# Kernel tuning notes

Hardware: AMD Instinct MI355X
Metric: run time of the kernel (lower is better)

The kernel has to match this reference:

```python
import jax, jax.numpy as jnp
import numpy as np

N, D, E = 16384, 256, 8
H = D // 2  # gate hidden


def setup_inputs() -> dict:
    key = jax.random.key(0)
    ks = jax.random.split(key, 10)
    s = lambda fan_in: 1.0 / np.sqrt(fan_in)
    return {
        "x":   jax.random.normal(ks[0], (N, D), dtype=jnp.float32),
        # gate: Linear(D, D//2) -> ReLU -> Linear(D//2, E) -> Softmax
        "Wg1": jax.random.uniform(ks[1], (D, H), jnp.float32, -s(D), s(D)),
        "bg1": jax.random.uniform(ks[2], (H,), jnp.float32, -s(D), s(D)),
        "Wg2": jax.random.uniform(ks[3], (H, E), jnp.float32, -s(H), s(H)),
        "bg2": jax.random.uniform(ks[4], (E,), jnp.float32, -s(H), s(H)),
        # experts: per-expert Linear(D,D) -> ReLU -> (Dropout eval=identity) -> Linear(D,D)
        "W1": jax.random.uniform(ks[5], (E, D, D), jnp.float32, -s(D), s(D)),
        "b1": jax.random.uniform(ks[6], (E, D), jnp.float32, -s(D), s(D)),
        "W2": jax.random.uniform(ks[7], (E, D, D), jnp.float32, -s(D), s(D)),
        "b2": jax.random.uniform(ks[8], (E, D), jnp.float32, -s(D), s(D)),
    }


def reference(x, Wg1, bg1, Wg2, bg2, W1, b1, W2, b2):
    # gate: [N, E] softmax over experts
    g = jax.nn.softmax(jax.nn.relu(x @ Wg1 + bg1) @ Wg2 + bg2, axis=-1)
    # all experts applied densely via batched GEMMs (fuses the Python loop)
    h = jax.nn.relu(jnp.einsum("nd,edh->neh", x, W1) + b1)  # [N, E, D]
    y = jnp.einsum("neh,ehd->ned", h, W2) + b2              # [N, E, D]
    # weighted combine: sum_e g[n,e] * y[n,e,:]
    return jnp.einsum("ned,ne->nd", y, g)
```

## Files before the change

### kernel.cpp

```cpp
#include <hip/hip_runtime.h>


typedef unsigned short USH;
typedef float f32x4 __attribute__((ext_vector_type(4)));
typedef __bf16 bf16x8 __attribute__((ext_vector_type(8)));

#define AS1 __attribute__((address_space(1)))
#define AS3 __attribute__((address_space(3)))

__device__ __forceinline__ USH f2bf(float f) {
  unsigned int u = __float_as_uint(f);
  u += 0x7fffu + ((u >> 16) & 1u);
  return (USH)(u >> 16);
}

__device__ __forceinline__ void gl2lds16(const void* g, void* l) {
  __builtin_amdgcn_global_load_lds((AS1 const void*)g, (AS3 void*)l, 16, 0, 0);
}


__global__ __launch_bounds__(256) void k_prep(
    const float* __restrict__ x,
    const float* __restrict__ Wg1,
    const float* __restrict__ W1,
    const float* __restrict__ W2,
    USH* __restrict__ xb, USH* __restrict__ wg1t,
    USH* __restrict__ w1f, USH* __restrict__ w2f) {
  __shared__ float T[64][65];
  int b = blockIdx.x, tid = threadIdx.x;

  if (b < 2048) {
    size_t i8 = ((size_t)b * 256 + tid) * 8;
    float4 a = *(const float4*)(x + i8);
    float4 c = *(const float4*)(x + i8 + 4);
    USH v[8];
    v[0] = f2bf(a.x); v[1] = f2bf(a.y); v[2] = f2bf(a.z); v[3] = f2bf(a.w);
    v[4] = f2bf(c.x); v[5] = f2bf(c.y); v[6] = f2bf(c.z); v[7] = f2bf(c.w);
    *(uint4*)(xb + i8) = *(const uint4*)v;
  } else if (b < 2176) {
    int bp = b - 2048;
    int e = bp >> 4, tl = bp & 15;
    int c0 = (tl >> 2) * 64, h0 = (tl & 3) * 64;
    const float* src = W1 + (size_t)e * 65536;
#pragma unroll
    for (int p = 0; p < 4; ++p) {
      int r = p * 16 + (tid >> 4), d4 = (tid & 15) * 4;
      float4 v = *(const float4*)(src + (size_t)(c0 + r) * 256 + h0 + d4);
      T[r][d4] = v.x; T[r][d4 + 1] = v.y; T[r][d4 + 2] = v.z; T[r][d4 + 3] = v.w;
    }
    __syncthreads();
#pragma unroll
    for (int p = 0; p < 4; ++p) {
      int hr = p * 16 + (tid >> 4), c4 = (tid & 15) * 4;
      USH w[4];
#pragma unroll
      for (int j = 0; j < 4; ++j) w[j] = f2bf(T[c4 + j][hr]);
      int h = h0 + hr;
      int t = h >> 4, lh = h & 15;
      int kt = c0 >> 6, ch = c4 >> 5, q = (c4 >> 3) & 3, u0 = c4 & 7;
      size_t idx = ((size_t)((e * 64 + kt * 16 + t) * 2 + ch)) * 512 + (q * 16 + lh) * 8 + u0;
      *(uint2*)(w1f + idx) = *(const uint2*)w;
    }
  } else if (b < 2184) {
    int bp = b - 2176;
    int c0 = (bp >> 1) * 64, h0 = (bp & 1) * 64;
#pragma unroll
    for (int p = 0; p < 4; ++p) {
      int r = p * 16 + (tid >> 4), d4 = (tid & 15) * 4;
      float4 v = *(const float4*)(Wg1 + (size_t)(c0 + r) * 128 + h0 + d4);
      T[r][d4] = v.x; T[r][d4 + 1] = v.y; T[r][d4 + 2] = v.z; T[r][d4 + 3] = v.w;
    }
    __syncthreads();
#pragma unroll
    for (int p = 0; p < 4; ++p) {
      int hr = p * 16 + (tid >> 4), c4 = (tid & 15) * 4;
      USH w[4];
#pragma unroll
      for (int j = 0; j < 4; ++j) w[j] = f2bf(T[c4 + j][hr]);
      *(uint2*)(wg1t + (size_t)(h0 + hr) * 256 + c0 + c4) = *(const uint2*)w;
    }
  } else {
    int bp = b - 2184;
    int e = bp >> 4, tl = bp & 15;
    int h0 = (tl >> 2) * 64, d0 = (tl & 3) * 64;
    const float* src = W2 + (size_t)e * 65536;
#pragma unroll
    for (int p = 0; p < 4; ++p) {
      int r = p * 16 + (tid >> 4), d4 = (tid & 15) * 4;
      float4 v = *(const float4*)(src + (size_t)(h0 + r) * 256 + d0 + d4);
      T[r][d4] = v.x; T[r][d4 + 1] = v.y; T[r][d4 + 2] = v.z; T[r][d4 + 3] = v.w;
    }
    __syncthreads();
#pragma unroll
    for (int p = 0; p < 4; ++p) {
      int dr = p * 16 + (tid >> 4), h4 = (tid & 15) * 4;
      USH w[4];
#pragma unroll
      for (int j = 0; j < 4; ++j) w[j] = f2bf(T[h4 + j][dr]);
      int d = d0 + dr;
      int t = d >> 4, ld = d & 15;
      int ht = h0 >> 6, ch = h4 >> 5, q = (h4 >> 3) & 3, u0 = h4 & 7;
      size_t idx = ((size_t)((e * 64 + ht * 16 + t) * 2 + ch)) * 512 + (q * 16 + ld) * 8 + u0;
      *(uint2*)(w2f + idx) = *(const uint2*)w;
    }
  }
}


__global__ __launch_bounds__(256) void k_gate(const USH* __restrict__ xb,
                                              const USH* __restrict__ wg1t,
                                              const float* __restrict__ bg1,
                                              const float* __restrict__ wg2,
                                              const float* __restrict__ bg2,
                                              float* __restrict__ g) {
  __shared__ __align__(16) USH As[32 * 64];
  __shared__ __align__(16) USH Bs[128 * 64];
  __shared__ float hg[32 * 129];
  __shared__ float bg1s[128];
  __shared__ float w2s[128 * 8];
  __shared__ float b2s[8];
  __shared__ float lg[32 * 8];

  int tid = threadIdx.x;
  int wave = tid >> 6, lane = tid & 63;
  int quad = lane >> 4, l16 = lane & 15;
  int sw = l16 & 7;
  int wr = wave >> 1, wc = wave & 1;
  int rowBase = blockIdx.x * 32;

  for (int t = tid; t < 1024; t += 256) w2s[t] = wg2[t];
  if (tid < 8) b2s[tid] = bg2[tid];
  if (tid < 128) bg1s[tid] = bg1[tid];

  f32x4 acc[4] = {};
  for (int kt = 0; kt < 4; ++kt) {
    int kb = kt * 64;
    {
      int r = tid >> 3, c8 = (tid & 7) ^ (r & 7);
      gl2lds16(xb + (size_t)(rowBase + r) * 256 + kb + c8 * 8, As + (size_t)tid * 8);
    }
#pragma unroll
    for (int c = 0; c < 4; ++c) {
      int i = c * 256 + tid;
      int r = i >> 3, c8 = (i & 7) ^ (r & 7);
      gl2lds16(wg1t + (size_t)r * 256 + kb + c8 * 8, Bs + (size_t)i * 8);
    }
    __syncthreads();
#pragma unroll
    for (int kkc = 0; kkc < 8; kkc += 4) {
      bf16x8 av = *(const bf16x8*)(As + (wr * 16 + l16) * 64 + (((kkc + quad) ^ sw) * 8));
#pragma unroll
      for (int j = 0; j < 4; ++j) {
        bf16x8 bv = *(const bf16x8*)(Bs + (wc * 64 + j * 16 + l16) * 64 + (((kkc + quad) ^ sw) * 8));
        acc[j] = __builtin_amdgcn_mfma_f32_16x16x32_bf16(av, bv, acc[j], 0, 0, 0);
      }
    }
    __syncthreads();
  }

#pragma unroll
  for (int j = 0; j < 4; ++j)
#pragma unroll
    for (int r = 0; r < 4; ++r) {
      int row = wr * 16 + quad * 4 + r;
      int col = wc * 64 + j * 16 + l16;
      hg[row * 129 + col] = fmaxf(acc[j][r] + bg1s[col], 0.0f);
    }
  __syncthreads();

  {
    int row = tid >> 3, p = tid & 7;
    float s = b2s[p];
    for (int k = 0; k < 128; ++k) s += hg[row * 129 + k] * w2s[k * 8 + p];
    lg[row * 8 + p] = s;
  }
  __syncthreads();

  if (tid < 32) {
    float l[8];
    float m = -1e30f;
#pragma unroll
    for (int e = 0; e < 8; ++e) { l[e] = lg[tid * 8 + e]; m = fmaxf(m, l[e]); }
    float s = 0.0f;
#pragma unroll
    for (int e = 0; e < 8; ++e) { l[e] = expf(l[e] - m); s += l[e]; }
    float inv = 1.0f / s;
    size_t grow = rowBase + tid;
#pragma unroll
    for (int e = 0; e < 8; ++e) g[grow * 8 + e] = l[e] * inv;
  }
}


__global__ __launch_bounds__(512) void k_moe(const USH* __restrict__ xb,
                                             const USH* __restrict__ w1f,
                                             const USH* __restrict__ w2f,
                                             const float* __restrict__ b1,
                                             const float* __restrict__ b2,
                                             const float* __restrict__ g,
                                             float* __restrict__ out) {
  __shared__ __align__(16) USH xs[4 * 64 * 64];
  __shared__ __align__(16) USH Hs[2][64 * 256];
  __shared__ float b1s[2048];
  __shared__ float b2s[2048];
  __shared__ float gse[512];

  int tid = threadIdx.x;
  int wave = tid >> 6, lane = tid & 63;
  int quad = lane >> 4, l16 = lane & 15;
  int sw = l16 & 7;
  int rowBase = blockIdx.x * 64;

#pragma unroll
  for (int it = 0; it < 4; ++it) {
    int i = it * 512 + tid;
    int kt = i >> 9, rem = i & 511;
    int r = rem >> 3, slot = rem & 7;
    int c8 = slot ^ (r & 7);
    gl2lds16(xb + (size_t)(rowBase + r) * 256 + kt * 64 + c8 * 8, xs + (size_t)i * 8);
  }

  bf16x8 wra[8], wrb[8];
  auto LDWH = [&](bf16x8* dst, const USH* We, int tb) {
#pragma unroll
    for (int k = 0; k < 2; ++k)
#pragma unroll
      for (int c = 0; c < 2; ++c)
#pragma unroll
        for (int i = 0; i < 2; ++i)
          dst[k * 4 + c * 2 + i] = *(const bf16x8*)(
              We + (size_t)(((tb + k) * 16 + wave * 2 + i) * 2 + c) * 512 + lane * 8);
  };
  LDWH(wra, w1f, 0);
  LDWH(wrb, w1f, 2);

#pragma unroll
  for (int t = 0; t < 4; ++t) {
    b1s[t * 512 + tid] = b1[t * 512 + tid];
    b2s[t * 512 + tid] = b2[t * 512 + tid];
  }
  {
    int e = tid >> 6, n = tid & 63;
    gse[tid] = g[(size_t)(rowBase + n) * 8 + e];
  }

  asm volatile("s_waitcnt vmcnt(0) lgkmcnt(0)" ::: "memory");
  __builtin_amdgcn_s_barrier();

  f32x4 oacc[4][2] = {};

#pragma unroll 1
  for (int e = 0; e < 8; ++e) {
    const USH* W2e = w2f + (size_t)e * 65536;
    const USH* W1n = w1f + (size_t)((e + 1) & 7) * 65536;
    f32x4 hacc[2][4] = {};

#pragma unroll
    for (int kt = 0; kt < 2; ++kt)
#pragma unroll
      for (int c = 0; c < 2; ++c) {
        int cs = ((c * 4 + quad) ^ sw) * 8;
        bf16x8 bv[4];
#pragma unroll
        for (int j = 0; j < 4; ++j)
          bv[j] = *(const bf16x8*)(xs + kt * 4096 + (j * 16 + l16) * 64 + cs);
#pragma unroll
        for (int i = 0; i < 2; ++i)
#pragma unroll
          for (int j = 0; j < 4; ++j)
            hacc[i][j] = __builtin_amdgcn_mfma_f32_16x16x32_bf16(
                wra[kt * 4 + c * 2 + i], bv[j], hacc[i][j], 0, 0, 0);
      }
    LDWH(wra, W2e, 0);
#pragma unroll
    for (int kt = 2; kt < 4; ++kt)
#pragma unroll
      for (int c = 0; c < 2; ++c) {
        int cs = ((c * 4 + quad) ^ sw) * 8;
        bf16x8 bv[4];
#pragma unroll
        for (int j = 0; j < 4; ++j)
          bv[j] = *(const bf16x8*)(xs + kt * 4096 + (j * 16 + l16) * 64 + cs);
#pragma unroll
        for (int i = 0; i < 2; ++i)
#pragma unroll
          for (int j = 0; j < 4; ++j)
            hacc[i][j] = __builtin_amdgcn_mfma_f32_16x16x32_bf16(
                wrb[(kt - 2) * 4 + c * 2 + i], bv[j], hacc[i][j], 0, 0, 0);
      }
    LDWH(wrb, W2e, 2);

    USH* Hb = &Hs[e & 1][0];
#pragma unroll
    for (int i = 0; i < 2; ++i) {
      int slot = (wave & 1) * 4 + i * 2 + (quad >> 1);
      int hb = wave * 32 + i * 16 + quad * 4;
#pragma unroll
      for (int j = 0; j < 4; ++j) {
        int n = j * 16 + l16;
        float gg = gse[e * 64 + n];
        USH w4[4];
#pragma unroll
        for (int r = 0; r < 4; ++r)
          w4[r] = f2bf(fmaxf(hacc[i][j][r] + b1s[e * 256 + hb + r], 0.0f) * gg);
        int off = n * 256 + (wave >> 1) * 64 + ((slot ^ (n & 7)) * 8) + (quad & 1) * 4;
        *(uint2*)(Hb + off) = *(const uint2*)w4;
      }
    }

    asm volatile("s_waitcnt lgkmcnt(0)" ::: "memory");
    __builtin_amdgcn_s_barrier();

#pragma unroll
    for (int ht = 0; ht < 2; ++ht)
#pragma unroll
      for (int c = 0; c < 2; ++c) {
        int cs = ((c * 4 + quad) ^ sw) * 8;
        bf16x8 av[4];
#pragma unroll
        for (int i = 0; i < 4; ++i)
          av[i] = *(const bf16x8*)(Hb + (i * 16 + l16) * 256 + ht * 64 + cs);
#pragma unroll
        for (int i = 0; i < 4; ++i)
#pragma unroll
          for (int j = 0; j < 2; ++j)
            oacc[i][j] = __builtin_amdgcn_mfma_f32_16x16x32_bf16(
                av[i], wra[ht * 4 + c * 2 + j], oacc[i][j], 0, 0, 0);
      }
    LDWH(wra, W1n, 0);
#pragma unroll
    for (int ht = 2; ht < 4; ++ht)
#pragma unroll
      for (int c = 0; c < 2; ++c) {
        int cs = ((c * 4 + quad) ^ sw) * 8;
        bf16x8 av[4];
#pragma unroll
        for (int i = 0; i < 4; ++i)
          av[i] = *(const bf16x8*)(Hb + (i * 16 + l16) * 256 + ht * 64 + cs);
#pragma unroll
        for (int i = 0; i < 4; ++i)
#pragma unroll
          for (int j = 0; j < 2; ++j)
            oacc[i][j] = __builtin_amdgcn_mfma_f32_16x16x32_bf16(
                av[i], wrb[(ht - 2) * 4 + c * 2 + j], oacc[i][j], 0, 0, 0);
      }
    LDWH(wrb, W1n, 2);
  }

#pragma unroll
  for (int i = 0; i < 4; ++i)
#pragma unroll
    for (int r = 0; r < 4; ++r) {
      int n = i * 16 + quad * 4 + r;
      size_t grow = (size_t)(rowBase + n) * 256;
#pragma unroll
      for (int j = 0; j < 2; ++j) {
        int d = wave * 32 + j * 16 + l16;
        float bias = 0.0f;
#pragma unroll
        for (int ee = 0; ee < 8; ++ee) bias += gse[ee * 64 + n] * b2s[ee * 256 + d];
        out[grow + d] = oacc[i][j][r] + bias;
      }
    }
}


extern "C" void kernel_launch(void* const* d_in, const int* in_sizes, int n_in,
                              void* d_out, int out_size, void* d_ws, size_t ws_size,
                              hipStream_t stream) {
  const float* x   = (const float*)d_in[0];
  const float* Wg1 = (const float*)d_in[1];
  const float* bg1 = (const float*)d_in[2];
  const float* Wg2 = (const float*)d_in[3];
  const float* bg2 = (const float*)d_in[4];
  const float* W1  = (const float*)d_in[5];
  const float* b1  = (const float*)d_in[6];
  const float* W2  = (const float*)d_in[7];
  const float* b2  = (const float*)d_in[8];
  float* out = (float*)d_out;

  char* ws = (char*)d_ws;
  USH*   xb  = (USH*)(ws);
  USH*   w1f = (USH*)(ws + 8388608);
  USH*   wg1t = (USH*)(ws + 9437184);
  USH*   w2f = (USH*)(ws + 9502720);
  float* g   = (float*)(ws + 10584064);

  hipLaunchKernelGGL(k_prep, dim3(2312), dim3(256), 0, stream,
                     x, Wg1, W1, W2, xb, wg1t, w1f, w2f);
  hipLaunchKernelGGL(k_gate, dim3(512), dim3(256), 0, stream,
                     xb, wg1t, bg1, Wg2, bg2, g);
  hipLaunchKernelGGL(k_moe, dim3(256), dim3(512), 0, stream,
                     xb, w1f, w2f, b1, b2, g, out);
}
```

Measured before the change: 130.6 us.

## Fuse gate network and x bf16 conversion into the MoE kernel

Result: faster. 123.2 us (-5.7%).

```diff
diff --git a/kernel.cpp b/kernel.cpp
--- a/kernel.cpp
+++ b/kernel.cpp
@@ -4,9 +4,6 @@
 typedef unsigned short USH;
 typedef float f32x4 __attribute__((ext_vector_type(4)));
 typedef __bf16 bf16x8 __attribute__((ext_vector_type(8)));
-
-#define AS1 __attribute__((address_space(1)))
-#define AS3 __attribute__((address_space(3)))
 
 __device__ __forceinline__ USH f2bf(float f) {
   unsigned int u = __float_as_uint(f);
@@ -14,32 +11,17 @@
   return (USH)(u >> 16);
 }
 
-__device__ __forceinline__ void gl2lds16(const void* g, void* l) {
-  __builtin_amdgcn_global_load_lds((AS1 const void*)g, (AS3 void*)l, 16, 0, 0);
-}
-
 
 __global__ __launch_bounds__(256) void k_prep(
-    const float* __restrict__ x,
     const float* __restrict__ Wg1,
     const float* __restrict__ W1,
     const float* __restrict__ W2,
-    USH* __restrict__ xb, USH* __restrict__ wg1t,
-    USH* __restrict__ w1f, USH* __restrict__ w2f) {
+    USH* __restrict__ w1f, USH* __restrict__ w2f, USH* __restrict__ wg1f) {
   __shared__ float T[64][65];
   int b = blockIdx.x, tid = threadIdx.x;
 
-  if (b < 2048) {
-    size_t i8 = ((size_t)b * 256 + tid) * 8;
-    float4 a = *(const float4*)(x + i8);
-    float4 c = *(const float4*)(x + i8 + 4);
-    USH v[8];
-    v[0] = f2bf(a.x); v[1] = f2bf(a.y); v[2] = f2bf(a.z); v[3] = f2bf(a.w);
-    v[4] = f2bf(c.x); v[5] = f2bf(c.y); v[6] = f2bf(c.z); v[7] = f2bf(c.w);
-    *(uint4*)(xb + i8) = *(const uint4*)v;
-  } else if (b < 2176) {
-    int bp = b - 2048;
-    int e = bp >> 4, tl = bp & 15;
+  if (b < 128) {
+    int e = b >> 4, tl = b & 15;
     int c0 = (tl >> 2) * 64, h0 = (tl & 3) * 64;
     const float* src = W1 + (size_t)e * 65536;
 #pragma unroll
@@ -57,12 +39,36 @@
       for (int j = 0; j < 4; ++j) w[j] = f2bf(T[c4 + j][hr]);
       int h = h0 + hr;
       int t = h >> 4, lh = h & 15;
-      int kt = c0 >> 6, ch = c4 >> 5, q = (c4 >> 3) & 3, u0 = c4 & 7;
+      int kt = c0 >> 6, ch = (c4 >> 5) & 1, q = (c4 >> 3) & 3, u0 = c4 & 7;
       size_t idx = ((size_t)((e * 64 + kt * 16 + t) * 2 + ch)) * 512 + (q * 16 + lh) * 8 + u0;
       *(uint2*)(w1f + idx) = *(const uint2*)w;
     }
-  } else if (b < 2184) {
-    int bp = b - 2176;
+  } else if (b < 256) {
+    int bp = b - 128;
+    int e = bp >> 4, tl = bp & 15;
+    int h0 = (tl >> 2) * 64, d0 = (tl & 3) * 64;
+    const float* src = W2 + (size_t)e * 65536;
+#pragma unroll
+    for (int p = 0; p < 4; ++p) {
+      int r = p * 16 + (tid >> 4), d4 = (tid & 15) * 4;
+      float4 v = *(const float4*)(src + (size_t)(h0 + r) * 256 + d0 + d4);
+      T[r][d4] = v.x; T[r][d4 + 1] = v.y; T[r][d4 + 2] = v.z; T[r][d4 + 3] = v.w;
+    }
+    __syncthreads();
+#pragma unroll
+    for (int p = 0; p < 4; ++p) {
+      int dr = p * 16 + (tid >> 4), h4 = (tid & 15) * 4;
+      USH w[4];
+#pragma unroll
+      for (int j = 0; j < 4; ++j) w[j] = f2bf(T[h4 + j][dr]);
+      int d = d0 + dr;
+      int t = d >> 4, ld = d & 15;
+      int ht = h0 >> 6, ch = (h4 >> 5) & 1, q = (h4 >> 3) & 3, u0 = h4 & 7;
+      size_t idx = ((size_t)((e * 64 + ht * 16 + t) * 2 + ch)) * 512 + (q * 16 + ld) * 8 + u0;
+      *(uint2*)(w2f + idx) = *(const uint2*)w;
+    }
+  } else {
+    int bp = b - 256;
     int c0 = (bp >> 1) * 64, h0 = (bp & 1) * 64;
 #pragma unroll
     for (int p = 0; p < 4; ++p) {
@@ -77,139 +83,42 @@
       USH w[4];
 #pragma unroll
       for (int j = 0; j < 4; ++j) w[j] = f2bf(T[c4 + j][hr]);
-      *(uint2*)(wg1t + (size_t)(h0 + hr) * 256 + c0 + c4) = *(const uint2*)w;
-    }
-  } else {
-    int bp = b - 2184;
-    int e = bp >> 4, tl = bp & 15;
-    int h0 = (tl >> 2) * 64, d0 = (tl & 3) * 64;
-    const float* src = W2 + (size_t)e * 65536;
-#pragma unroll
-    for (int p = 0; p < 4; ++p) {
-      int r = p * 16 + (tid >> 4), d4 = (tid & 15) * 4;
-      float4 v = *(const float4*)(src + (size_t)(h0 + r) * 256 + d0 + d4);
-      T[r][d4] = v.x; T[r][d4 + 1] = v.y; T[r][d4 + 2] = v.z; T[r][d4 + 3] = v.w;
-    }
-    __syncthreads();
-#pragma unroll
-    for (int p = 0; p < 4; ++p) {
-      int dr = p * 16 + (tid >> 4), h4 = (tid & 15) * 4;
-      USH w[4];
-#pragma unroll
-      for (int j = 0; j < 4; ++j) w[j] = f2bf(T[h4 + j][dr]);
-      int d = d0 + dr;
-      int t = d >> 4, ld = d & 15;
-      int ht = h0 >> 6, ch = h4 >> 5, q = (h4 >> 3) & 3, u0 = h4 & 7;
-      size_t idx = ((size_t)((e * 64 + ht * 16 + t) * 2 + ch)) * 512 + (q * 16 + ld) * 8 + u0;
-      *(uint2*)(w2f + idx) = *(const uint2*)w;
+      int h = h0 + hr;
+      int t = h >> 4, lh = h & 15;
+      int kt = c0 >> 6, ch = (c4 >> 5) & 1, q = (c4 >> 3) & 3, u0 = c4 & 7;
+      size_t idx = ((size_t)((kt * 8 + t) * 2 + ch)) * 512 + (q * 16 + lh) * 8 + u0;
+      *(uint2*)(wg1f + idx) = *(const uint2*)w;
     }
   }
 }
 
 
-__global__ __launch_bounds__(256) void k_gate(const USH* __restrict__ xb,
-                                              const USH* __restrict__ wg1t,
-                                              const float* __restrict__ bg1,
-                                              const float* __restrict__ wg2,
-                                              const float* __restrict__ bg2,
-                                              float* __restrict__ g) {
-  __shared__ __align__(16) USH As[32 * 64];
-  __shared__ __align__(16) USH Bs[128 * 64];
-  __shared__ float hg[32 * 129];
-  __shared__ float bg1s[128];
-  __shared__ float w2s[128 * 8];
-  __shared__ float b2s[8];
-  __shared__ float lg[32 * 8];
-
-  int tid = threadIdx.x;
-  int wave = tid >> 6, lane = tid & 63;
-  int quad = lane >> 4, l16 = lane & 15;
-  int sw = l16 & 7;
-  int wr = wave >> 1, wc = wave & 1;
-  int rowBase = blockIdx.x * 32;
-
-  for (int t = tid; t < 1024; t += 256) w2s[t] = wg2[t];
-  if (tid < 8) b2s[tid] = bg2[tid];
-  if (tid < 128) bg1s[tid] = bg1[tid];
-
-  f32x4 acc[4] = {};
-  for (int kt = 0; kt < 4; ++kt) {
-    int kb = kt * 64;
-    {
-      int r = tid >> 3, c8 = (tid & 7) ^ (r & 7);
-      gl2lds16(xb + (size_t)(rowBase + r) * 256 + kb + c8 * 8, As + (size_t)tid * 8);
-    }
-#pragma unroll
-    for (int c = 0; c < 4; ++c) {
-      int i = c * 256 + tid;
-      int r = i >> 3, c8 = (i & 7) ^ (r & 7);
-      gl2lds16(wg1t + (size_t)r * 256 + kb + c8 * 8, Bs + (size_t)i * 8);
-    }
-    __syncthreads();
-#pragma unroll
-    for (int kkc = 0; kkc < 8; kkc += 4) {
-      bf16x8 av = *(const bf16x8*)(As + (wr * 16 + l16) * 64 + (((kkc + quad) ^ sw) * 8));
-#pragma unroll
-      for (int j = 0; j < 4; ++j) {
-        bf16x8 bv = *(const bf16x8*)(Bs + (wc * 64 + j * 16 + l16) * 64 + (((kkc + quad) ^ sw) * 8));
-        acc[j] = __builtin_amdgcn_mfma_f32_16x16x32_bf16(av, bv, acc[j], 0, 0, 0);
-      }
-    }
-    __syncthreads();
-  }
-
-#pragma unroll
-  for (int j = 0; j < 4; ++j)
-#pragma unroll
-    for (int r = 0; r < 4; ++r) {
-      int row = wr * 16 + quad * 4 + r;
-      int col = wc * 64 + j * 16 + l16;
-      hg[row * 129 + col] = fmaxf(acc[j][r] + bg1s[col], 0.0f);
-    }
-  __syncthreads();
-
-  {
-    int row = tid >> 3, p = tid & 7;
-    float s = b2s[p];
-    for (int k = 0; k < 128; ++k) s += hg[row * 129 + k] * w2s[k * 8 + p];
-    lg[row * 8 + p] = s;
-  }
-  __syncthreads();
-
-  if (tid < 32) {
-    float l[8];
-    float m = -1e30f;
-#pragma unroll
-    for (int e = 0; e < 8; ++e) { l[e] = lg[tid * 8 + e]; m = fmaxf(m, l[e]); }
-    float s = 0.0f;
-#pragma unroll
-    for (int e = 0; e < 8; ++e) { l[e] = expf(l[e] - m); s += l[e]; }
-    float inv = 1.0f / s;
-    size_t grow = rowBase + tid;
-#pragma unroll
-    for (int e = 0; e < 8; ++e) g[grow * 8 + e] = l[e] * inv;
-  }
-}
-
-
-__global__ __launch_bounds__(512) void k_moe(const USH* __restrict__ xb,
+__global__ __launch_bounds__(512) void k_moe(const float* __restrict__ x,
                                              const USH* __restrict__ w1f,
                                              const USH* __restrict__ w2f,
+                                             const USH* __restrict__ wg1f,
+                                             const float* __restrict__ wg2,
+                                             const float* __restrict__ bg1,
+                                             const float* __restrict__ bg2,
                                              const float* __restrict__ b1,
                                              const float* __restrict__ b2,
-                                             const float* __restrict__ g,
                                              float* __restrict__ out) {
   __shared__ __align__(16) USH xs[4 * 64 * 64];
   __shared__ __align__(16) USH Hs[2][64 * 256];
   __shared__ float b1s[2048];
   __shared__ float b2s[2048];
   __shared__ float gse[512];
+  __shared__ float wg2t[8 * 132];
+  __shared__ float lgg[512];
+  __shared__ float bg1s[128];
+  __shared__ float bg2g[8];
 
   int tid = threadIdx.x;
   int wave = tid >> 6, lane = tid & 63;
   int quad = lane >> 4, l16 = lane & 15;
   int sw = l16 & 7;
   int rowBase = blockIdx.x * 64;
+  float* hgs = (float*)&Hs[0][0];
 
 #pragma unroll
   for (int it = 0; it < 4; ++it) {
@@ -217,8 +126,22 @@
     int kt = i >> 9, rem = i & 511;
     int r = rem >> 3, slot = rem & 7;
     int c8 = slot ^ (r & 7);
-    gl2lds16(xb + (size_t)(rowBase + r) * 256 + kt * 64 + c8 * 8, xs + (size_t)i * 8);
-  }
+    const float* sp = x + (size_t)(rowBase + r) * 256 + kt * 64 + c8 * 8;
+    float4 a = *(const float4*)sp;
+    float4 bq = *(const float4*)(sp + 4);
+    USH v[8];
+    v[0] = f2bf(a.x);  v[1] = f2bf(a.y);  v[2] = f2bf(a.z);  v[3] = f2bf(a.w);
+    v[4] = f2bf(bq.x); v[5] = f2bf(bq.y); v[6] = f2bf(bq.z); v[7] = f2bf(bq.w);
+    *(uint4*)(xs + (size_t)i * 8) = *(const uint4*)v;
+  }
+#pragma unroll
+  for (int t = 0; t < 4; ++t) {
+    b1s[t * 512 + tid] = b1[t * 512 + tid];
+    b2s[t * 512 + tid] = b2[t * 512 + tid];
+  }
+  for (int t = tid; t < 1024; t += 512) wg2t[(t & 7) * 132 + (t >> 3)] = wg2[t];
+  if (tid < 128) bg1s[tid] = bg1[tid];
+  if (tid < 8) bg2g[tid] = bg2[tid];
 
   bf16x8 wra[8], wrb[8];
   auto LDWH = [&](bf16x8* dst, const USH* We, int tb) {
@@ -234,17 +157,67 @@
   LDWH(wra, w1f, 0);
   LDWH(wrb, w1f, 2);
 
-#pragma unroll
-  for (int t = 0; t < 4; ++t) {
-    b1s[t * 512 + tid] = b1[t * 512 + tid];
-    b2s[t * 512 + tid] = b2[t * 512 + tid];
-  }
+  asm volatile("s_waitcnt lgkmcnt(0)" ::: "memory");
+  __builtin_amdgcn_s_barrier();
+
   {
-    int e = tid >> 6, n = tid & 63;
-    gse[tid] = g[(size_t)(rowBase + n) * 8 + e];
-  }
-
-  asm volatile("s_waitcnt vmcnt(0) lgkmcnt(0)" ::: "memory");
+    f32x4 hg4[4] = {};
+#pragma unroll
+    for (int kt = 0; kt < 4; ++kt)
+#pragma unroll
+      for (int c = 0; c < 2; ++c) {
+        int cs = ((c * 4 + quad) ^ sw) * 8;
+        bf16x8 av = *(const bf16x8*)(wg1f + (size_t)((kt * 8 + wave) * 2 + c) * 512 + lane * 8);
+        bf16x8 bv[4];
+#pragma unroll
+        for (int j = 0; j < 4; ++j)
+          bv[j] = *(const bf16x8*)(xs + kt * 4096 + (j * 16 + l16) * 64 + cs);
+#pragma unroll
+        for (int j = 0; j < 4; ++j)
+          hg4[j] = __builtin_amdgcn_mfma_f32_16x16x32_bf16(av, bv[j], hg4[j], 0, 0, 0);
+      }
+    int hb = wave * 16 + quad * 4;
+    int slotbase = wave * 4 + quad;
+#pragma unroll
+    for (int j = 0; j < 4; ++j) {
+      int n = j * 16 + l16;
+      int slot = slotbase ^ (n & 7);
+      f32x4 v;
+#pragma unroll
+      for (int r = 0; r < 4; ++r) v[r] = fmaxf(hg4[j][r] + bg1s[hb + r], 0.0f);
+      *(f32x4*)(hgs + n * 128 + slot * 4) = v;
+    }
+  }
+  asm volatile("s_waitcnt lgkmcnt(0)" ::: "memory");
+  __builtin_amdgcn_s_barrier();
+
+  {
+    int n = tid >> 3, eg = tid & 7;
+    float s = bg2g[eg];
+#pragma unroll
+    for (int k4 = 0; k4 < 32; ++k4) {
+      int slot = k4 ^ (n & 7);
+      f32x4 hv = *(const f32x4*)(hgs + n * 128 + slot * 4);
+      const float* wv = wg2t + eg * 132 + k4 * 4;
+      s += hv[0] * wv[0]; s += hv[1] * wv[1]; s += hv[2] * wv[2]; s += hv[3] * wv[3];
+    }
+    lgg[tid] = s;
+  }
+  asm volatile("s_waitcnt lgkmcnt(0)" ::: "memory");
+  __builtin_amdgcn_s_barrier();
+
+  if (tid < 64) {
+    float l[8]; float m = -1e30f;
+#pragma unroll
+    for (int e = 0; e < 8; ++e) { l[e] = lgg[tid * 8 + e]; m = fmaxf(m, l[e]); }
+    float s = 0.0f;
+#pragma unroll
+    for (int e = 0; e < 8; ++e) { l[e] = expf(l[e] - m); s += l[e]; }
+    float inv = 1.0f / s;
+#pragma unroll
+    for (int e = 0; e < 8; ++e) gse[e * 64 + tid] = l[e] * inv;
+  }
+  asm volatile("s_waitcnt lgkmcnt(0)" ::: "memory");
   __builtin_amdgcn_s_barrier();
 
   f32x4 oacc[4][2] = {};
@@ -380,16 +353,12 @@
   float* out = (float*)d_out;
 
   char* ws = (char*)d_ws;
-  USH*   xb  = (USH*)(ws);
-  USH*   w1f = (USH*)(ws + 8388608);
-  USH*   wg1t = (USH*)(ws + 9437184);
-  USH*   w2f = (USH*)(ws + 9502720);
-  float* g   = (float*)(ws + 10584064);
-
-  hipLaunchKernelGGL(k_prep, dim3(2312), dim3(256), 0, stream,
-                     x, Wg1, W1, W2, xb, wg1t, w1f, w2f);
-  hipLaunchKernelGGL(k_gate, dim3(512), dim3(256), 0, stream,
-                     xb, wg1t, bg1, Wg2, bg2, g);
+  USH* w1f  = (USH*)(ws + 8388608);
+  USH* wg1f = (USH*)(ws + 9437184);
+  USH* w2f  = (USH*)(ws + 9502720);
+
+  hipLaunchKernelGGL(k_prep, dim3(264), dim3(256), 0, stream,
+                     Wg1, W1, W2, w1f, w2f, wg1f);
   hipLaunchKernelGGL(k_moe, dim3(256), dim3(512), 0, stream,
-                     xb, w1f, w2f, b1, b2, g, out);
+                     x, w1f, w2f, wg1f, Wg2, bg1, bg2, b1, b2, out);
 }
```
